# Kernel tuning notes

Hardware: AMD Instinct MI355X
Metric: run time of the kernel (lower is better)

The kernel has to match this reference:

```python
import jax, jax.numpy as jnp
import numpy as np

EPS = 1e-7  # tf.keras.backend.epsilon()
ROUTING_ITERS = 3


def setup_inputs() -> dict:
    key = jax.random.key(0)
    k1, k2 = jax.random.split(key)
    B, I, Din = 64, 4096, 8
    N, D = 10, 16
    inputs = jax.random.normal(k1, (B, I, Din), dtype=jnp.float32)
    # glorot_uniform-ish init for W [I, N, Din, D]
    limit = (6.0 / (Din + D)) ** 0.5
    W = jax.random.uniform(k2, (I, N, Din, D), dtype=jnp.float32, minval=-limit, maxval=limit)
    return {"inputs": inputs, "W": W}


def _elementwise_squash(s):
    # Original squashes over axis=-2 of [B,1,N,1,D], a size-1 axis ->
    # the reduce_sum is a no-op and squash becomes elementwise.
    sq = s * s
    scale = sq / (1.0 + sq) / jnp.sqrt(sq + EPS)
    return scale * s


def reference(inputs, W):
    # inputs: [B, I, Din], W: [I, N, Din, D]
    # u_hat[b,i,n,d] = sum_p inputs[b,i,p] * W[i,n,p,d]  (the tile+matmul)
    u_hat = jnp.einsum('bip,inpd->bind', inputs, W)  # [B, I, N, D]
    B, I, N, D = u_hat.shape
    b = jnp.zeros((B, I, N, 1), dtype=u_hat.dtype)
    v = None
    for it in range(ROUTING_ITERS):
        c = jax.nn.softmax(b, axis=2)                 # [B, I, N, 1]
        s = jnp.sum(c * u_hat, axis=1)                # [B, N, D]
        v = _elementwise_squash(s)                    # [B, N, D]
        if it < ROUTING_ITERS - 1:
            # agreement: sum over D -> [B, I, N, 1]
            b = b + jnp.sum(u_hat * v[:, None, :, :], axis=-1, keepdims=True)
    # original: squeeze(v[B,1,N,1,D], axis=1) -> [B, N, 1, D]
    return v[:, :, None, :]
```

## Files before the change

kernel.cpp:

```cpp
#include <hip/hip_runtime.h>
#include <math.h>

#define B_ 64
#define I_ 4096
#define P_ 8
#define N_ 10
#define D_ 16
#define ND_ 160
#define BND_ (B_*ND_)
#define PSTR_ 10304
#define EPS_ 1e-7f

#define IPB_ 8
#define NBLK_ (I_ / IPB_)
#define WTILE_ (N_ * P_ * D_)
#define NSTR_ 144
#define ILSTR_ (N_ * NSTR_)
#define XSTR_ 68

#define NGRP_ 16
#define GSZ_  32
#define LINEW_ 16
#define SLOTW_ ((NGRP_ + 1) * LINEW_)
#define NSLOT_ 5

template<int CTRL>
__device__ __forceinline__ float dpp_bcast(float v) {
    int r = __builtin_amdgcn_update_dpp(0, __float_as_int(v), CTRL, 0xF, 0xF, true);
    return __int_as_float(r);
}

__device__ __forceinline__ void agent_store_f2(float* dst, float a, float b) {
    float2 v; v.x = a; v.y = b;
    unsigned long long u; __builtin_memcpy(&u, &v, 8);
    __hip_atomic_store((unsigned long long*)dst, u,
                       __ATOMIC_RELAXED, __HIP_MEMORY_SCOPE_AGENT);
}
__device__ __forceinline__ float2 agent_load_f2(const float* src) {
    unsigned long long u = __hip_atomic_load((unsigned long long*)src,
                       __ATOMIC_RELAXED, __HIP_MEMORY_SCOPE_AGENT);
    float2 v; __builtin_memcpy(&v, &u, 8); return v;
}
__device__ __forceinline__ void agent_store_f(float* dst, float v) {
    __hip_atomic_store(dst, v, __ATOMIC_RELAXED, __HIP_MEMORY_SCOPE_AGENT);
}

__device__ __forceinline__ unsigned gridbar_arrive(unsigned* cnt, int slot) {
    __syncthreads();
    unsigned epoch = 0;
    if (threadIdx.x == 0) {
        unsigned* base = cnt + slot * SLOTW_;
        const unsigned g = (unsigned)blockIdx.x & (NGRP_ - 1u);
        unsigned* gl = base + g * LINEW_;
        unsigned* rp = base + NGRP_ * LINEW_;
        __builtin_amdgcn_fence(__ATOMIC_RELEASE, "workgroup");
        unsigned gold = __hip_atomic_fetch_add(&gl[0], 1u,
                            __ATOMIC_RELAXED, __HIP_MEMORY_SCOPE_AGENT);
        epoch = gold / (unsigned)GSZ_;
        if ((gold % (unsigned)GSZ_) == (unsigned)GSZ_ - 1u)
            __hip_atomic_fetch_add(&rp[0], 1u,
                __ATOMIC_RELAXED, __HIP_MEMORY_SCOPE_AGENT);
    }
    return epoch;
}

__device__ __forceinline__ void gridbar_wait(unsigned* cnt, int slot, unsigned epoch) {
    if (threadIdx.x == 0) {
        unsigned* base = cnt + slot * SLOTW_;
        const unsigned g = (unsigned)blockIdx.x & (NGRP_ - 1u);
        unsigned* gl = base + g * LINEW_;
        unsigned* rp = base + NGRP_ * LINEW_;
        long long t0 = (long long)__builtin_amdgcn_s_memrealtime();
        if ((unsigned)blockIdx.x < (unsigned)NGRP_) {
            unsigned rtgt = (epoch + 1u) * (unsigned)NGRP_;
            while (__hip_atomic_load(&rp[0], __ATOMIC_RELAXED,
                                     __HIP_MEMORY_SCOPE_AGENT) < rtgt) {
                __builtin_amdgcn_s_sleep(1);
                if ((long long)__builtin_amdgcn_s_memrealtime() - t0 > 2000000LL)
                    break;
            }
            __hip_atomic_store(&gl[1], epoch + 1u,
                __ATOMIC_RELAXED, __HIP_MEMORY_SCOPE_AGENT);
        } else {
            while (__hip_atomic_load(&gl[1], __ATOMIC_RELAXED,
                                     __HIP_MEMORY_SCOPE_AGENT) < epoch + 1u) {
                __builtin_amdgcn_s_sleep(1);
                if ((long long)__builtin_amdgcn_s_memrealtime() - t0 > 2000000LL)
                    break;
            }
        }
        __builtin_amdgcn_fence(__ATOMIC_ACQUIRE, "workgroup");
    }
    __syncthreads();
}

__global__ __launch_bounds__(256, 2)
void digitcaps_fused(const float* __restrict__ x, const float* __restrict__ W,
                     float* __restrict__ part, float* __restrict__ Vc,
                     float* __restrict__ out, unsigned* __restrict__ cnt)
{
    __shared__ float wsh[IPB_ * ILSTR_];
    __shared__ float xsh[B_ * XSTR_];
    __shared__ float4 rsm4[32][5];
    const int t = threadIdx.x;
    const int lane = t & 63;
    const int ds  = lane & 7;
    const int np  = (lane >> 3) & 1;
    const int bl2 = lane >> 4;
    const int wv  = t >> 6;
    const int bb  = wv * 16 + bl2 * 4;
    const int i0  = blockIdx.x * IPB_;

    {
        const float4* __restrict__ Wg = (const float4*)(W + (size_t)i0 * WTILE_);
        float4* __restrict__ Ws = (float4*)wsh;
#pragma unroll
        for (int c0 = 0; c0 < (IPB_ * WTILE_) / (4 * 256); ++c0) {
            int c  = c0 * 256 + t;
            int il = c / 320;
            int r  = c - il * 320;
            int n  = r >> 5;
            int s  = r & 31;
            Ws[il * 360 + n * 36 + s] = Wg[c];
        }
    }
    {
        const int xb = t >> 2;
        const int xc = t & 3;
        const float4* __restrict__ xg = (const float4*)(x + ((size_t)xb * I_ + i0) * P_);
        float4* __restrict__ xd = (float4*)(xsh + xb * XSTR_);
#pragma unroll
        for (int q = 0; q < 4; ++q)
            xd[xc * 4 + q] = xg[xc * 4 + q];
    }
    __syncthreads();

    auto compute_tv = [&](int il, float (&tv)[4][5][2]) {
        const float* __restrict__ Wb = wsh + il * ILSTR_ + np * NSTR_ + 2 * ds;
        float xr[4][P_];
#pragma unroll
        for (int j = 0; j < 4; ++j) {
            const float4* xp = (const float4*)(xsh + (bb + j) * XSTR_ + il * P_);
            float4 a0 = xp[0], a1 = xp[1];
            xr[j][0]=a0.x; xr[j][1]=a0.y; xr[j][2]=a0.z; xr[j][3]=a0.w;
            xr[j][4]=a1.x; xr[j][5]=a1.y; xr[j][6]=a1.z; xr[j][7]=a1.w;
        }
#pragma unroll
        for (int k = 0; k < 5; ++k) {
#pragma unroll
            for (int j = 0; j < 4; ++j) { tv[j][k][0] = 0.f; tv[j][k][1] = 0.f; }
#pragma unroll
            for (int p = 0; p < P_; ++p) {
                float2 w = *(const float2*)(Wb + k * 2 * NSTR_ + p * D_);
#pragma unroll
                for (int j = 0; j < 4; ++j) {
                    tv[j][k][0] = fmaf(w.x, xr[j][p], tv[j][k][0]);
                    tv[j][k][1] = fmaf(w.y, xr[j][p], tv[j][k][1]);
                }
            }
        }
    };

    float vprev = 0.f;
    unsigned epO = 0;

    for (int it = 0; it < 3; ++it) {
        const bool uni = (it == 0);

        float acc[4][5][2];
#pragma unroll
        for (int j = 0; j < 4; ++j)
#pragma unroll
            for (int k = 0; k < 5; ++k) { acc[j][k][0] = 0.f; acc[j][k][1] = 0.f; }

        float vc[4][5][2];
        float tv[4][5][2];

        compute_tv(0, tv);
        if (!uni) {
            gridbar_wait(cnt, (it - 1) * 2 + 1, epO);
#pragma unroll
            for (int j = 0; j < 4; ++j)
#pragma unroll
                for (int k = 0; k < 5; ++k) {
                    float2 v = agent_load_f2(Vc + (size_t)(bb + j) * ND_
                                             + (np + 2 * k) * D_ + 2 * ds);
                    vc[j][k][0] = v.x; vc[j][k][1] = v.y;
                }
        }

#pragma unroll 1
        for (int il = 0; il < IPB_; ++il) {
            if (il > 0) compute_tv(il, tv);

            if (uni) {
#pragma unroll
                for (int j = 0; j < 4; ++j)
#pragma unroll
                    for (int k = 0; k < 5; ++k) {
                        acc[j][k][0] += tv[j][k][0];
                        acc[j][k][1] += tv[j][k][1];
                    }
            } else {
#pragma unroll
                for (int j = 0; j < 4; ++j) {
                    float e[5];
                    float m = -1e30f;
#pragma unroll
                    for (int k = 0; k < 5; ++k) {
                        float l = fmaf(tv[j][k][1], vc[j][k][1],
                                       tv[j][k][0] * vc[j][k][0]);
                        l += dpp_bcast<0xB1>(l);
                        l += dpp_bcast<0x4E>(l);
                        l += dpp_bcast<0x141>(l);
                        e[k] = l;
                        m = fmaxf(m, l);
                    }
                    m = fmaxf(m, dpp_bcast<0x140>(m));
                    float se = 0.f;
#pragma unroll
                    for (int k = 0; k < 5; ++k) { e[k] = __expf(e[k] - m); se += e[k]; }
                    se += dpp_bcast<0x140>(se);
                    float inv = 1.f / se;
#pragma unroll
                    for (int k = 0; k < 5; ++k) {
                        float cn = e[k] * inv;
                        acc[j][k][0] = fmaf(cn, tv[j][k][0], acc[j][k][0]);
                        acc[j][k][1] = fmaf(cn, tv[j][k][1], acc[j][k][1]);
                    }
                }
            }
        }

#pragma unroll
        for (int j = 0; j < 4; ++j) {
            float* __restrict__ dst = part + (size_t)blockIdx.x * PSTR_
                                      + (size_t)(bb + j) * ND_ + np * D_ + 2 * ds;
#pragma unroll
            for (int k = 0; k < 5; ++k)
                agent_store_f2(dst + k * 2 * D_, acc[j][k][0], acc[j][k][1]);
        }

        {
            unsigned epE = gridbar_arrive(cnt, it * 2);
            gridbar_wait(cnt, it * 2, epE);
        }

        const int o0 = blockIdx.x * 20;
        if (t < 160) {
            const int fg = t % 5;
            const int tp = t / 5;
            const float* __restrict__ p0 = part + (size_t)(tp * 16) * PSTR_
                                           + o0 + fg * 4;
            float2 va[32];
#pragma unroll
            for (int r = 0; r < 16; ++r) {
                va[2*r]   = agent_load_f2(p0 + (size_t)r * PSTR_);
                va[2*r+1] = agent_load_f2(p0 + (size_t)r * PSTR_ + 2);
            }
            float4 s4 = {0.f, 0.f, 0.f, 0.f};
#pragma unroll
            for (int r = 0; r < 16; ++r) {
                s4.x += va[2*r].x;   s4.y += va[2*r].y;
                s4.z += va[2*r+1].x; s4.w += va[2*r+1].y;
            }
            rsm4[tp][fg] = s4;
        }
        __syncthreads();
        if (t < 20) {
            const int fg = t >> 2, c = t & 3;
            float tot = 0.f;
#pragma unroll
            for (int tp = 0; tp < 32; ++tp)
                tot += ((const float*)&rsm4[tp][fg])[c];
            tot *= uni ? 0.1f : 1.0f;
            float sq = tot * tot;
            float v = tot * (sq / ((1.f + sq) * sqrtf(sq + EPS_)));
            const int o2 = o0 + t;
            if (it == 0)      { vprev = v;   agent_store_f(Vc + o2, vprev); }
            else if (it == 1) { vprev += v;  agent_store_f(Vc + o2, vprev); }
            else              out[o2] = v;
        }

        if (it < 2) epO = gridbar_arrive(cnt, it * 2 + 1);
    }
}

extern "C" void kernel_launch(void* const* d_in, const int* in_sizes, int n_in,
                              void* d_out, int out_size, void* d_ws, size_t ws_size,
                              hipStream_t stream)
{
    const float* x = (const float*)d_in[0];
    const float* W = (const float*)d_in[1];
    float* out = (float*)d_out;

    float* part = (float*)d_ws;
    float* Vc   = part + (size_t)NBLK_ * PSTR_;
    unsigned* cnt = (unsigned*)(Vc + BND_);

    hipMemsetAsync(cnt, 0, NSLOT_ * SLOTW_ * sizeof(unsigned), stream);

    digitcaps_fused<<<dim3(NBLK_), dim3(256), 0, stream>>>(x, W, part, Vc, out, cnt);
}
```

Measured before the change: 171.9 us.

## Halve capsules per block to double grid and occupancy, split x reads

Each block now handles 4 input capsules instead of 8. That doubles the number of blocks and shrinks shared memory, so launch bounds ask for 4 blocks per CU. The per-block reduction now covers 10 outputs and reads each partial-sum column over 64 slices in two batches, and the x tile is staged in two halves to lower register pressure. The intent is more resident waves and better latency hiding. The cost is twice as many partial-sum rows to reduce and more blocks taking part in every grid barrier.

```diff
diff --git a/kernel.cpp b/kernel.cpp
--- a/kernel.cpp
+++ b/kernel.cpp
@@ -11,15 +11,15 @@
 #define PSTR_ 10304
 #define EPS_ 1e-7f
 
-#define IPB_ 8
+#define IPB_ 4
 #define NBLK_ (I_ / IPB_)
 #define WTILE_ (N_ * P_ * D_)
 #define NSTR_ 144
 #define ILSTR_ (N_ * NSTR_)
-#define XSTR_ 68
+#define XSTR_ 36
 
 #define NGRP_ 16
-#define GSZ_  32
+#define GSZ_  64
 #define LINEW_ 16
 #define SLOTW_ ((NGRP_ + 1) * LINEW_)
 #define NSLOT_ 5
@@ -94,14 +94,14 @@
     __syncthreads();
 }
 
-__global__ __launch_bounds__(256, 2)
+__global__ __launch_bounds__(256, 4)
 void digitcaps_fused(const float* __restrict__ x, const float* __restrict__ W,
                      float* __restrict__ part, float* __restrict__ Vc,
                      float* __restrict__ out, unsigned* __restrict__ cnt)
 {
     __shared__ float wsh[IPB_ * ILSTR_];
     __shared__ float xsh[B_ * XSTR_];
-    __shared__ float4 rsm4[32][5];
+    __shared__ float2 rsm2[32][5];
     const int t = threadIdx.x;
     const int lane = t & 63;
     const int ds  = lane & 7;
@@ -130,34 +130,36 @@
         const float4* __restrict__ xg = (const float4*)(x + ((size_t)xb * I_ + i0) * P_);
         float4* __restrict__ xd = (float4*)(xsh + xb * XSTR_);
 #pragma unroll
-        for (int q = 0; q < 4; ++q)
-            xd[xc * 4 + q] = xg[xc * 4 + q];
+        for (int q = 0; q < 2; ++q)
+            xd[xc * 2 + q] = xg[xc * 2 + q];
     }
     __syncthreads();
 
     auto compute_tv = [&](int il, float (&tv)[4][5][2]) {
         const float* __restrict__ Wb = wsh + il * ILSTR_ + np * NSTR_ + 2 * ds;
-        float xr[4][P_];
-#pragma unroll
-        for (int j = 0; j < 4; ++j) {
-            const float4* xp = (const float4*)(xsh + (bb + j) * XSTR_ + il * P_);
-            float4 a0 = xp[0], a1 = xp[1];
-            xr[j][0]=a0.x; xr[j][1]=a0.y; xr[j][2]=a0.z; xr[j][3]=a0.w;
-            xr[j][4]=a1.x; xr[j][5]=a1.y; xr[j][6]=a1.z; xr[j][7]=a1.w;
-        }
-#pragma unroll
-        for (int k = 0; k < 5; ++k) {
+#pragma unroll
+        for (int k = 0; k < 5; ++k)
 #pragma unroll
             for (int j = 0; j < 4; ++j) { tv[j][k][0] = 0.f; tv[j][k][1] = 0.f; }
 #pragma unroll
-            for (int p = 0; p < P_; ++p) {
-                float2 w = *(const float2*)(Wb + k * 2 * NSTR_ + p * D_);
-#pragma unroll
-                for (int j = 0; j < 4; ++j) {
-                    tv[j][k][0] = fmaf(w.x, xr[j][p], tv[j][k][0]);
-                    tv[j][k][1] = fmaf(w.y, xr[j][p], tv[j][k][1]);
+        for (int ph = 0; ph < 2; ++ph) {
+            float xr[4][4];
+#pragma unroll
+            for (int j = 0; j < 4; ++j) {
+                float4 a = *(const float4*)(xsh + (bb + j) * XSTR_ + il * P_ + ph * 4);
+                xr[j][0]=a.x; xr[j][1]=a.y; xr[j][2]=a.z; xr[j][3]=a.w;
+            }
+#pragma unroll
+            for (int k = 0; k < 5; ++k)
+#pragma unroll
+                for (int p = 0; p < 4; ++p) {
+                    float2 w = *(const float2*)(Wb + k * 2 * NSTR_ + (ph * 4 + p) * D_);
+#pragma unroll
+                    for (int j = 0; j < 4; ++j) {
+                        tv[j][k][0] = fmaf(w.x, xr[j][p], tv[j][k][0]);
+                        tv[j][k][1] = fmaf(w.y, xr[j][p], tv[j][k][1]);
+                    }
                 }
-            }
         }
     };
 
@@ -246,33 +248,31 @@
             gridbar_wait(cnt, it * 2, epE);
         }
 
-        const int o0 = blockIdx.x * 20;
+        const int o0 = blockIdx.x * 10;
         if (t < 160) {
             const int fg = t % 5;
             const int tp = t / 5;
-            const float* __restrict__ p0 = part + (size_t)(tp * 16) * PSTR_
-                                           + o0 + fg * 4;
-            float2 va[32];
-#pragma unroll
-            for (int r = 0; r < 16; ++r) {
-                va[2*r]   = agent_load_f2(p0 + (size_t)r * PSTR_);
-                va[2*r+1] = agent_load_f2(p0 + (size_t)r * PSTR_ + 2);
-            }
-            float4 s4 = {0.f, 0.f, 0.f, 0.f};
-#pragma unroll
-            for (int r = 0; r < 16; ++r) {
-                s4.x += va[2*r].x;   s4.y += va[2*r].y;
-                s4.z += va[2*r+1].x; s4.w += va[2*r+1].y;
-            }
-            rsm4[tp][fg] = s4;
+            float2 s2 = {0.f, 0.f};
+#pragma unroll
+            for (int bat = 0; bat < 2; ++bat) {
+                const float* __restrict__ p0 = part
+                    + (size_t)(tp * 32 + bat * 16) * PSTR_ + o0 + fg * 2;
+                float2 va[16];
+#pragma unroll
+                for (int r = 0; r < 16; ++r)
+                    va[r] = agent_load_f2(p0 + (size_t)r * PSTR_);
+#pragma unroll
+                for (int r = 0; r < 16; ++r) { s2.x += va[r].x; s2.y += va[r].y; }
+            }
+            rsm2[tp][fg] = s2;
         }
         __syncthreads();
-        if (t < 20) {
-            const int fg = t >> 2, c = t & 3;
+        if (t < 10) {
+            const int fg = t >> 1, c = t & 1;
             float tot = 0.f;
 #pragma unroll
             for (int tp = 0; tp < 32; ++tp)
-                tot += ((const float*)&rsm4[tp][fg])[c];
+                tot += c ? rsm2[tp][fg].y : rsm2[tp][fg].x;
             tot *= uni ? 0.1f : 1.0f;
             float sq = tot * tot;
             float v = tot * (sq / ((1.f + sq) * sqrtf(sq + EPS_)));
```

After: 382.6 us. 2.23x slower.
